# Kernel tuning notes

Hardware: AMD Instinct MI355X
Metric: run time of the kernel (lower is better)

Reference implementation:

```python
import jax, jax.numpy as jnp
import numpy as np

NUM_HEADS = 12

def setup_inputs() -> dict:
    key = jax.random.key(0)
    ks = jax.random.split(key, 8)
    B, N, C = 8, 1024, 768
    s = 1.0 / np.sqrt(C)
    return {
        "x": jax.random.normal(ks[0], (B, N, C), jnp.float32),
        "head_mask": jnp.ones((B, NUM_HEADS), jnp.float32),
        "q_w": jax.random.normal(ks[1], (C, C), jnp.float32) * s,
        "q_b": jnp.zeros((C,), jnp.float32),
        "k_w": jax.random.normal(ks[2], (C, C), jnp.float32) * s,
        "k_b": jnp.zeros((C,), jnp.float32),
        "v_w": jax.random.normal(ks[3], (C, C), jnp.float32) * s,
        "v_b": jnp.zeros((C,), jnp.float32),
        "proj_w": jax.random.normal(ks[4], (C, C), jnp.float32) * s,
        "proj_b": jnp.zeros((C,), jnp.float32),
    }

def reference(x, head_mask, q_w, q_b, k_w, k_b, v_w, v_b, proj_w, proj_b):
    B, N, C = x.shape
    H = NUM_HEADS
    d = C // H
    scale = d ** -0.5
    # torch Linear: y = x @ W.T + b; reshape to [B,H,N,d]
    q = (x @ q_w.T + q_b).reshape(B, N, H, d).transpose(0, 2, 1, 3)
    k = (x @ k_w.T + k_b).reshape(B, N, H, d).transpose(0, 2, 1, 3)
    v = (x @ v_w.T + v_b).reshape(B, N, H, d).transpose(0, 2, 1, 3)
    attn = jnp.einsum('bhnd,bhmd->bhnm', q, k) * scale
    attn = jax.nn.softmax(attn, axis=-1)
    y = jnp.einsum('bhnm,bhmd->bhnd', attn, v)
    # head_mask applied per head [B,H,1,1]
    y = y * head_mask[:, :, None, None]
    out = y.transpose(0, 2, 1, 3).reshape(B, N, C)
    # head_mask repeated per head_dim, applied to flattened channels [B,1,C]
    hm_flat = jnp.repeat(head_mask, d, axis=1)[:, None, :]
    out = out * hm_flat
    return out @ proj_w.T + proj_b
```

## Files before the change

### kernel.cpp

```cpp
#include <hip/hip_runtime.h>

typedef _Float16 half_t;
typedef _Float16 half2_t __attribute__((ext_vector_type(2)));
typedef _Float16 half4_t __attribute__((ext_vector_type(4)));
typedef _Float16 half8 __attribute__((ext_vector_type(8)));
typedef float f32x4 __attribute__((ext_vector_type(4)));
typedef float f32x16 __attribute__((ext_vector_type(16)));
typedef unsigned uint4v __attribute__((ext_vector_type(4)));

__device__ __forceinline__ void gload_lds16(const void* g, void* l) {
    __builtin_amdgcn_global_load_lds(
        (const __attribute__((address_space(1))) void*)g,
        (__attribute__((address_space(3))) void*)l, 16, 0, 0);
}

__global__ __launch_bounds__(256) void megacast(const float* __restrict__ x,
                                                const float* __restrict__ w0,
                                                const float* __restrict__ w1,
                                                const float* __restrict__ w2,
                                                const float* __restrict__ w3,
                                                const float* __restrict__ b0,
                                                const float* __restrict__ b1,
                                                const float* __restrict__ b2,
                                                half_t* __restrict__ xh,
                                                half_t* __restrict__ wc,
                                                float* __restrict__ bc) {
    const int tid = blockIdx.x * blockDim.x + threadIdx.x;
    if (tid < 2304) bc[tid] = tid < 768 ? b0[tid] : tid < 1536 ? b1[tid - 768] : b2[tid - 1536];
    const int stride = gridDim.x * blockDim.x;
    for (long i = tid; i < 2162688; i += stride) {
        const float* s;
        half_t* d;
        long off;
        if (i < 1572864) { s = x; d = xh; off = i; }
        else {
            const long j = i - 1572864;
            const int which = (int)(j / 147456);
            off = j - (long)which * 147456;
            s = which == 0 ? w0 : which == 1 ? w1 : which == 2 ? w2 : w3;
            d = wc + (long)which * 589824;
        }
        const float4 v = *(const float4*)(s + off * 4);
        half4_t h = {(half_t)v.x, (half_t)v.y, (half_t)v.z, (half_t)v.w};
        *(half4_t*)(d + off * 4) = h;
    }
}

template <typename OutT, bool VSPLIT>
__global__ __launch_bounds__(256) void gemm128(const half_t* __restrict__ A,
                                               const half_t* __restrict__ W,
                                               const float* __restrict__ bias,
                                               OutT* __restrict__ C,
                                               half_t* __restrict__ Vt,
                                               const int N) {
    constexpr int Kdim = 768, NT = 12;
    alignas(16) __shared__ half_t Ah[2][128 * 64];
    alignas(16) __shared__ half_t Wh[2][128 * 64];

    const int t = threadIdx.x, l = t & 63, wv = t >> 6;
    const int wr = wv >> 1, wc = wv & 1;
    const int m0 = blockIdx.x * 128, n0 = blockIdx.y * 128;

    f32x4 acc[4][4] = {};

    const int srow_g = wv * 8 + (l >> 3);
    const int schunk = l & 7;

    const half_t* Ag = A + (long)m0 * Kdim;
    const half_t* Wg = W + (long)n0 * Kdim;

    auto STAGE = [&](int tile, int buf) {
        const int k0 = tile * 64;
#pragma unroll
        for (int g = 0; g < 4; ++g) {
            const int row = g * 32 + srow_g;
            const int sc_ = (schunk ^ (row & 7)) * 8;
            gload_lds16(Ag + (long)row * Kdim + k0 + sc_,
                        &Ah[buf][(g * 32 + wv * 8) * 64]);
            gload_lds16(Wg + (long)row * Kdim + k0 + sc_,
                        &Wh[buf][(g * 32 + wv * 8) * 64]);
        }
    };

    STAGE(0, 0);
    STAGE(1, 1);

    for (int tt = 0; tt < NT; ++tt) {
        const int buf = tt & 1;
        if (tt < NT - 1) {
            asm volatile("s_waitcnt vmcnt(8)" ::: "memory");
        } else {
            asm volatile("s_waitcnt vmcnt(0)" ::: "memory");
        }
        __builtin_amdgcn_s_barrier();
        asm volatile("" ::: "memory");

#pragma unroll
        for (int ks = 0; ks < 2; ++ks) {
            const int kc = ks * 4 + (l >> 4);
            half8 afr[4], bfr[4];
#pragma unroll
            for (int i = 0; i < 4; ++i) {
                const int arow = wr * 64 + i * 16 + (l & 15);
                afr[i] = *(const half8*)&Ah[buf][arow * 64 + (kc ^ (arow & 7)) * 8];
                const int brow = wc * 64 + i * 16 + (l & 15);
                bfr[i] = *(const half8*)&Wh[buf][brow * 64 + (kc ^ (brow & 7)) * 8];
            }
            __builtin_amdgcn_s_setprio(1);
#pragma unroll
            for (int mi = 0; mi < 4; ++mi)
#pragma unroll
                for (int ni = 0; ni < 4; ++ni)
                    acc[mi][ni] = __builtin_amdgcn_mfma_f32_16x16x32_f16(
                        afr[mi], bfr[ni], acc[mi][ni], 0, 0, 0);
            __builtin_amdgcn_s_setprio(0);
        }

        asm volatile("" ::: "memory");
        __builtin_amdgcn_s_barrier();
        if (tt + 2 < NT) STAGE(tt + 2, buf);
    }

    const bool vtile = VSPLIT && (blockIdx.y >= 12);
#pragma unroll
    for (int ni = 0; ni < 4; ++ni) {
        const int col = n0 + wc * 64 + ni * 16 + (l & 15);
        const float bb = bias[col];
        if (!vtile) {
#pragma unroll
            for (int mi = 0; mi < 4; ++mi) {
                const int row = m0 + wr * 64 + mi * 16 + (l >> 4) * 4;
#pragma unroll
                for (int r = 0; r < 4; ++r)
                    C[(long)(row + r) * N + col] = (OutT)(acc[mi][ni][r] + bb);
            }
        } else {
            const int hd = col - 1536;
            const int hidx = hd >> 6, d = hd & 63;
#pragma unroll
            for (int mi = 0; mi < 4; ++mi) {
                const int row = m0 + wr * 64 + mi * 16 + (l >> 4) * 4;
                const int b = row >> 10, n = row & 1023;
                const int np = (n & ~12) | ((n & 4) << 1) | ((n & 8) >> 1);
                half4_t pk;
#pragma unroll
                for (int r = 0; r < 4; ++r) pk[r] = (half_t)(acc[mi][ni][r] + bb);
                *(half4_t*)(Vt + ((long)((b * 12 + hidx) * 64 + d)) * 1024 + np) = pk;
            }
        }
    }
}

__global__ __launch_bounds__(256) void attn6_kernel(const half_t* __restrict__ qkv,
                                                    const half_t* __restrict__ Vt,
                                                    const float* __restrict__ head_mask,
                                                    half_t* __restrict__ Y) {
    alignas(16) __shared__ half_t Kl[2][64 * 64];
    alignas(16) __shared__ half_t Vl[2][64 * 64];

    const int t = threadIdx.x, l = t & 63, wv = t >> 6;
    const int h2 = l >> 5, q32 = l & 31;
    const int bh = blockIdx.x, b = bh / 12, hh = bh % 12;
    const int q0 = blockIdx.y * 128 + wv * 32;

    half8 qf[4];
    {
        const half_t SC = (half_t)(0.125f * 1.44269504f);
        const half_t* Qp = qkv + ((long)(b * 1024 + q0 + q32)) * 2304 + hh * 64 + h2 * 8;
#pragma unroll
        for (int kd = 0; kd < 4; ++kd) {
            half8 v = *(const half8*)(Qp + kd * 16);
#pragma unroll
            for (int j = 0; j < 8; ++j) v[j] = v[j] * SC;
            qf[kd] = v;
        }
    }

    const half8 ONES = {(half_t)1, (half_t)1, (half_t)1, (half_t)1,
                        (half_t)1, (half_t)1, (half_t)1, (half_t)1};

    const half_t* Kg = qkv + (long)b * 1024 * 2304 + 768 + hh * 64;
    const half_t* Vg = Vt + (long)bh * 64 * 1024;

    const int srow_lo = (l >> 3);
    const int schunk = l & 7;

    auto STAGE = [&](int tile, int bf) {
#pragma unroll
        for (int c = 0; c < 2; ++c) {
            const int row = c * 32 + wv * 8 + srow_lo;
            const int sc_ = (schunk ^ (row & 7)) * 8;
            gload_lds16(Kg + (long)(tile * 64 + row) * 2304 + sc_,
                        &Kl[bf][(c * 32 + wv * 8) * 64]);
            gload_lds16(Vg + (long)row * 1024 + tile * 64 + sc_,
                        &Vl[bf][(c * 32 + wv * 8) * 64]);
        }
    };

    f32x16 o0 = {}, o1 = {}, lacc = {};

    STAGE(0, 0);

    for (int tt = 0; tt < 16; ++tt) {
        const int bf = tt & 1;
        if (tt < 15) {
            STAGE(tt + 1, bf ^ 1);
            asm volatile("s_waitcnt vmcnt(4)" ::: "memory");
        } else {
            asm volatile("s_waitcnt vmcnt(0)" ::: "memory");
        }
        __builtin_amdgcn_s_barrier();
        asm volatile("" ::: "memory");

        f32x16 s0 = {}, s1 = {};
        __builtin_amdgcn_s_setprio(1);
#pragma unroll
        for (int kd = 0; kd < 4; ++kd) {
            const int ch = ((kd * 2 + h2) ^ (q32 & 7)) * 8;
            half8 k0 = *(const half8*)&Kl[bf][q32 * 64 + ch];
            half8 k1 = *(const half8*)&Kl[bf][(32 + q32) * 64 + ch];
            s0 = __builtin_amdgcn_mfma_f32_32x32x16_f16(k0, qf[kd], s0, 0, 0, 0);
            s1 = __builtin_amdgcn_mfma_f32_32x32x16_f16(k1, qf[kd], s1, 0, 0, 0);
        }
        __builtin_amdgcn_s_setprio(0);

#pragma unroll
        for (int kc = 0; kc < 4; ++kc) {
            const f32x16& ss = (kc >> 1) ? s1 : s0;
            const int rb = (kc & 1) * 8;
            unsigned pw[4];
#pragma unroll
            for (int k2 = 0; k2 < 4; ++k2) {
                const float a = __builtin_amdgcn_exp2f(ss[rb + 2 * k2]);
                const float c = __builtin_amdgcn_exp2f(ss[rb + 2 * k2 + 1]);
                pw[k2] = __builtin_bit_cast(unsigned, __builtin_amdgcn_cvt_pkrtz(a, c));
            }
            uint4v uu = {pw[0], pw[1], pw[2], pw[3]};
            const half8 pf = __builtin_bit_cast(half8, uu);

            const int ch = ((2 * kc + h2) ^ (q32 & 7)) * 8;
            half8 vf0 = *(const half8*)&Vl[bf][q32 * 64 + ch];
            half8 vf1 = *(const half8*)&Vl[bf][(32 + q32) * 64 + ch];

            __builtin_amdgcn_s_setprio(1);
            o0 = __builtin_amdgcn_mfma_f32_32x32x16_f16(vf0, pf, o0, 0, 0, 0);
            o1 = __builtin_amdgcn_mfma_f32_32x32x16_f16(vf1, pf, o1, 0, 0, 0);
            lacc = __builtin_amdgcn_mfma_f32_32x32x16_f16(ONES, pf, lacc, 0, 0, 0);
            __builtin_amdgcn_s_setprio(0);
        }

        asm volatile("" ::: "memory");
        __builtin_amdgcn_s_barrier();
    }

    const float hmv = head_mask[b * 12 + hh];
    const float sc = hmv * hmv / lacc[0];
    half_t* Yp = Y + ((long)(b * 1024 + q0 + q32)) * 768 + hh * 64;
#pragma unroll
    for (int db = 0; db < 2; ++db) {
        const f32x16 oo = db ? o1 : o0;
#pragma unroll
        for (int rq = 0; rq < 4; ++rq) {
            half4_t pk;
#pragma unroll
            for (int i = 0; i < 4; ++i) pk[i] = (half_t)(oo[rq * 4 + i] * sc);
            *(half4_t*)(Yp + db * 32 + rq * 8 + h2 * 4) = pk;
        }
    }
}

extern "C" void kernel_launch(void* const* d_in, const int* in_sizes, int n_in,
                              void* d_out, int out_size, void* d_ws, size_t ws_size,
                              hipStream_t stream) {
    const float* x   = (const float*)d_in[0];
    const float* hm  = (const float*)d_in[1];
    const float* q_w = (const float*)d_in[2];
    const float* q_b = (const float*)d_in[3];
    const float* k_w = (const float*)d_in[4];
    const float* k_b = (const float*)d_in[5];
    const float* v_w = (const float*)d_in[6];
    const float* v_b = (const float*)d_in[7];
    const float* p_w = (const float*)d_in[8];
    const float* p_b = (const float*)d_in[9];
    float* out = (float*)d_out;

    char* ws = (char*)d_ws;
    half_t* xh  = (half_t*)(ws);
    half_t* wc  = (half_t*)(ws + 12582912);
    half_t* pwh = (half_t*)(ws + 16121856);
    float*  bc  = (float*)(ws + 17301504);
    half_t* qkv = (half_t*)(ws + 17310720);
    half_t* y   = (half_t*)(ws + 55059456);
    half_t* Vt = (ws_size >= (size_t)67642368 + 12582912)
                     ? (half_t*)(ws + 67642368)
                     : (half_t*)d_out;

    megacast<<<2048, 256, 0, stream>>>(x, q_w, k_w, v_w, p_w, q_b, k_b, v_b, xh, wc, bc);

    gemm128<half_t, true><<<dim3(64, 18), 256, 0, stream>>>(xh, wc, bc, qkv, Vt, 2304);
    attn6_kernel<<<dim3(96, 8), 256, 0, stream>>>(qkv, Vt, hm, y);
    gemm128<float, false><<<dim3(64, 6), 256, 0, stream>>>(y, pwh, p_b, out, nullptr, 768);
}
```

Baseline: 109.2 us.

## Use 256x256 8-wave QKV GEMM with fine-grained phased prefetch

Replaces the 128x128 QKV projection GEMM with a 256x256-tile, 512-thread kernel. It splits each K tile into four quarter phases, interleaving half-tile async LDS loads with MFMA work between barriers and reusing B fragments across phases. The larger tile cuts global and LDS traffic per FLOP, but the grid drops to 288 blocks on 256 CUs, which risks poor wave balance and occupancy. The output projection GEMM is specialized to float output and loses its setprio hints.

```diff
diff --git a/kernel.cpp b/kernel.cpp
--- a/kernel.cpp
+++ b/kernel.cpp
@@ -1,7 +1,6 @@
 #include <hip/hip_runtime.h>
 
 typedef _Float16 half_t;
-typedef _Float16 half2_t __attribute__((ext_vector_type(2)));
 typedef _Float16 half4_t __attribute__((ext_vector_type(4)));
 typedef _Float16 half8 __attribute__((ext_vector_type(8)));
 typedef float f32x4 __attribute__((ext_vector_type(4)));
@@ -13,6 +12,10 @@
         (const __attribute__((address_space(1))) void*)g,
         (__attribute__((address_space(3))) void*)l, 16, 0, 0);
 }
+
+#define BARRIER() do { asm volatile("" ::: "memory"); \
+    __builtin_amdgcn_s_barrier(); asm volatile("" ::: "memory"); } while (0)
+#define VMW(n) asm volatile("s_waitcnt vmcnt(" #n ")" ::: "memory")
 
 __global__ __launch_bounds__(256) void megacast(const float* __restrict__ x,
                                                 const float* __restrict__ w0,
@@ -46,14 +49,124 @@
     }
 }
 
-template <typename OutT, bool VSPLIT>
-__global__ __launch_bounds__(256) void gemm128(const half_t* __restrict__ A,
-                                               const half_t* __restrict__ W,
-                                               const float* __restrict__ bias,
-                                               OutT* __restrict__ C,
-                                               half_t* __restrict__ Vt,
-                                               const int N) {
-    constexpr int Kdim = 768, NT = 12;
+__global__ __launch_bounds__(512) void gemm8x(const half_t* __restrict__ A,
+                                              const half_t* __restrict__ W,
+                                              const float* __restrict__ bias,
+                                              half_t* __restrict__ qkv,
+                                              half_t* __restrict__ Vt) {
+    alignas(16) __shared__ half_t As[2][2][128][64];
+    alignas(16) __shared__ half_t Bs[2][2][128][64];
+
+    const int t = threadIdx.x, l = t & 63, wv = t >> 6;
+    const int wr = wv >> 2, wc = wv & 3;
+    const int m0 = blockIdx.x * 256, n0 = blockIdx.y * 256;
+
+    f32x4 acc[8][4] = {};
+
+    auto SH = [&](int tile, int isB, int half) {
+        const half_t* G = (isB ? W + (long)(n0 + half * 128) * 768
+                               : A + (long)(m0 + half * 128) * 768);
+        half_t* dst = isB ? &Bs[tile & 1][half][0][0] : &As[tile & 1][half][0][0];
+#pragma unroll
+        for (int r = 0; r < 2; ++r) {
+            const int row = r * 64 + wv * 8 + (l >> 3);
+            const int c = (l & 7) ^ (row & 7);
+            gload_lds16(G + (long)row * 768 + tile * 64 + c * 8,
+                        dst + (r * 64 + wv * 8) * 64);
+        }
+    };
+
+    half8 bfr[8];
+
+#define PH(TILE, Q, LOADB, STAGE) do {                                          \
+    const int par_ = (TILE) & 1;                                                \
+    if (LOADB) {                                                                \
+        _Pragma("unroll") for (int ni = 0; ni < 4; ++ni)                        \
+        _Pragma("unroll") for (int s = 0; s < 2; ++s) {                         \
+            const int rowh = (wc & 1) * 64 + ni * 16 + (l & 15);                \
+            const int kc = s * 4 + (l >> 4);                                    \
+            bfr[ni * 2 + s] =                                                   \
+                *(const half8*)&Bs[par_][wc >> 1][rowh][(kc ^ (rowh & 7)) * 8]; \
+        }                                                                       \
+    }                                                                           \
+    half8 afr[2][2];                                                            \
+    _Pragma("unroll") for (int m2 = 0; m2 < 2; ++m2)                            \
+    _Pragma("unroll") for (int s = 0; s < 2; ++s) {                             \
+        const int rowh = ((Q) * 2 + m2) * 16 + (l & 15);                        \
+        const int kc = s * 4 + (l >> 4);                                        \
+        afr[m2][s] = *(const half8*)&As[par_][wr][rowh][(kc ^ (rowh & 7)) * 8]; \
+    }                                                                           \
+    STAGE;                                                                      \
+    __builtin_amdgcn_s_setprio(1);                                              \
+    _Pragma("unroll") for (int m2 = 0; m2 < 2; ++m2)                            \
+    _Pragma("unroll") for (int ni = 0; ni < 4; ++ni)                            \
+    _Pragma("unroll") for (int s = 0; s < 2; ++s)                               \
+        acc[(Q) * 2 + m2][ni] = __builtin_amdgcn_mfma_f32_16x16x32_f16(         \
+            afr[m2][s], bfr[ni * 2 + s], acc[(Q) * 2 + m2][ni], 0, 0, 0);       \
+    __builtin_amdgcn_s_setprio(0);                                              \
+} while (0)
+
+    SH(0, 0, 0); SH(0, 0, 1); SH(0, 1, 0); SH(0, 1, 1);
+    SH(1, 1, 0); SH(1, 1, 1);
+
+    for (int it = 0; it < 6; ++it) {
+        const int T = 2 * it;
+        const bool g2 = (T + 2 < 12), g3 = (T + 3 < 12);
+        VMW(4); BARRIER();
+        PH(T, 0, true,  SH(T + 1, 0, 0));
+        BARRIER();
+        PH(T, 1, false, SH(T + 1, 0, 1));
+        BARRIER();
+        PH(T, 2, false, if (g2) SH(T + 2, 1, 0));
+        BARRIER();
+        PH(T, 3, false, if (g2) SH(T + 2, 1, 1));
+        if (it < 5) { VMW(4); } else { VMW(0); }
+        BARRIER();
+        PH(T + 1, 0, true,  if (g2) SH(T + 2, 0, 0));
+        BARRIER();
+        PH(T + 1, 1, false, if (g2) SH(T + 2, 0, 1));
+        BARRIER();
+        PH(T + 1, 2, false, if (g3) SH(T + 3, 1, 0));
+        BARRIER();
+        PH(T + 1, 3, false, if (g3) SH(T + 3, 1, 1));
+    }
+#undef PH
+
+    const bool vtile = (blockIdx.y >= 6);
+#pragma unroll
+    for (int ni = 0; ni < 4; ++ni) {
+        const int col = n0 + wc * 64 + ni * 16 + (l & 15);
+        const float bb = bias[col];
+        if (!vtile) {
+#pragma unroll
+            for (int mi = 0; mi < 8; ++mi) {
+                const int row = m0 + wr * 128 + mi * 16 + (l >> 4) * 4;
+#pragma unroll
+                for (int r = 0; r < 4; ++r)
+                    qkv[(long)(row + r) * 2304 + col] = (half_t)(acc[mi][ni][r] + bb);
+            }
+        } else {
+            const int hd = col - 1536;
+            const int hidx = hd >> 6, d = hd & 63;
+#pragma unroll
+            for (int mi = 0; mi < 8; ++mi) {
+                const int row = m0 + wr * 128 + mi * 16 + (l >> 4) * 4;
+                const int b = row >> 10, n = row & 1023;
+                const int np = (n & ~12) | ((n & 4) << 1) | ((n & 8) >> 1);
+                half4_t pk;
+#pragma unroll
+                for (int r = 0; r < 4; ++r) pk[r] = (half_t)(acc[mi][ni][r] + bb);
+                *(half4_t*)(Vt + ((long)((b * 12 + hidx) * 64 + d)) * 1024 + np) = pk;
+            }
+        }
+    }
+}
+
+__global__ __launch_bounds__(256) void gemm128p(const half_t* __restrict__ A,
+                                                const half_t* __restrict__ W,
+                                                const float* __restrict__ bias,
+                                                float* __restrict__ C) {
+    constexpr int Kdim = 768, NT = 12, N = 768;
     alignas(16) __shared__ half_t Ah[2][128 * 64];
     alignas(16) __shared__ half_t Wh[2][128 * 64];
 
@@ -87,13 +200,8 @@
 
     for (int tt = 0; tt < NT; ++tt) {
         const int buf = tt & 1;
-        if (tt < NT - 1) {
-            asm volatile("s_waitcnt vmcnt(8)" ::: "memory");
-        } else {
-            asm volatile("s_waitcnt vmcnt(0)" ::: "memory");
-        }
-        __builtin_amdgcn_s_barrier();
-        asm volatile("" ::: "memory");
+        if (tt < NT - 1) { VMW(8); } else { VMW(0); }
+        BARRIER();
 
 #pragma unroll
         for (int ks = 0; ks < 2; ++ks) {
@@ -106,47 +214,28 @@
                 const int brow = wc * 64 + i * 16 + (l & 15);
                 bfr[i] = *(const half8*)&Wh[buf][brow * 64 + (kc ^ (brow & 7)) * 8];
             }
-            __builtin_amdgcn_s_setprio(1);
 #pragma unroll
             for (int mi = 0; mi < 4; ++mi)
 #pragma unroll
                 for (int ni = 0; ni < 4; ++ni)
                     acc[mi][ni] = __builtin_amdgcn_mfma_f32_16x16x32_f16(
                         afr[mi], bfr[ni], acc[mi][ni], 0, 0, 0);
-            __builtin_amdgcn_s_setprio(0);
-        }
-
-        asm volatile("" ::: "memory");
-        __builtin_amdgcn_s_barrier();
+        }
+
+        BARRIER();
         if (tt + 2 < NT) STAGE(tt + 2, buf);
     }
 
-    const bool vtile = VSPLIT && (blockIdx.y >= 12);
 #pragma unroll
     for (int ni = 0; ni < 4; ++ni) {
         const int col = n0 + wc * 64 + ni * 16 + (l & 15);
         const float bb = bias[col];
-        if (!vtile) {
-#pragma unroll
-            for (int mi = 0; mi < 4; ++mi) {
-                const int row = m0 + wr * 64 + mi * 16 + (l >> 4) * 4;
-#pragma unroll
-                for (int r = 0; r < 4; ++r)
-                    C[(long)(row + r) * N + col] = (OutT)(acc[mi][ni][r] + bb);
-            }
-        } else {
-            const int hd = col - 1536;
-            const int hidx = hd >> 6, d = hd & 63;
-#pragma unroll
-            for (int mi = 0; mi < 4; ++mi) {
-                const int row = m0 + wr * 64 + mi * 16 + (l >> 4) * 4;
-                const int b = row >> 10, n = row & 1023;
-                const int np = (n & ~12) | ((n & 4) << 1) | ((n & 8) >> 1);
-                half4_t pk;
-#pragma unroll
-                for (int r = 0; r < 4; ++r) pk[r] = (half_t)(acc[mi][ni][r] + bb);
-                *(half4_t*)(Vt + ((long)((b * 12 + hidx) * 64 + d)) * 1024 + np) = pk;
-            }
+#pragma unroll
+        for (int mi = 0; mi < 4; ++mi) {
+            const int row = m0 + wr * 64 + mi * 16 + (l >> 4) * 4;
+#pragma unroll
+            for (int r = 0; r < 4; ++r)
+                C[(long)(row + r) * N + col] = acc[mi][ni][r] + bb;
         }
     }
 }
@@ -205,12 +294,11 @@
         const int bf = tt & 1;
         if (tt < 15) {
             STAGE(tt + 1, bf ^ 1);
-            asm volatile("s_waitcnt vmcnt(4)" ::: "memory");
+            VMW(4);
         } else {
-            asm volatile("s_waitcnt vmcnt(0)" ::: "memory");
-        }
-        __builtin_amdgcn_s_barrier();
-        asm volatile("" ::: "memory");
+            VMW(0);
+        }
+        BARRIER();
 
         f32x16 s0 = {}, s1 = {};
         __builtin_amdgcn_s_setprio(1);
@@ -249,8 +337,7 @@
             __builtin_amdgcn_s_setprio(0);
         }
 
-        asm volatile("" ::: "memory");
-        __builtin_amdgcn_s_barrier();
+        BARRIER();
     }
 
     const float hmv = head_mask[b * 12 + hh];
@@ -297,7 +384,7 @@
 
     megacast<<<2048, 256, 0, stream>>>(x, q_w, k_w, v_w, p_w, q_b, k_b, v_b, xh, wc, bc);
 
-    gemm128<half_t, true><<<dim3(64, 18), 256, 0, stream>>>(xh, wc, bc, qkv, Vt, 2304);
+    gemm8x<<<dim3(32, 9), 512, 0, stream>>>(xh, wc, bc, qkv, Vt);
     attn6_kernel<<<dim3(96, 8), 256, 0, stream>>>(qkv, Vt, hm, y);
-    gemm128<float, false><<<dim3(64, 6), 256, 0, stream>>>(y, pwh, p_b, out, nullptr, 768);
-}
+    gemm128p<<<dim3(64, 6), 256, 0, stream>>>(y, pwh, p_b, out);
+}
```

Result: slower. 134.6 us (+23.3%).
